# Performance work log

Measured on AMD Instinct MI355X. Metric: run time of the kernel, lower is better.

## Reference

```python
import jax, jax.numpy as jnp
import numpy as np

N_NODES = 100000
N_EDGES = 1600000
IN_F = 128
OUT_F = 32


def setup_inputs() -> dict:
    key = jax.random.key(0)
    k1, k2, k3 = jax.random.split(key, 3)
    x = jax.random.normal(k1, (N_NODES, IN_F), dtype=jnp.float32)
    edge_index = jax.random.randint(k2, (2, N_EDGES), 0, N_NODES, dtype=jnp.int64)
    W = jax.random.normal(k3, (OUT_F, IN_F), dtype=jnp.float32) * 0.1
    b = jnp.zeros((OUT_F,), dtype=jnp.float32)
    return {"x": x, "edge_index": edge_index, "W": W, "b": b}


def reference(x, edge_index, W, b):
    # PyG GCNConv: add self-loops, symmetric normalization, linear, aggregate, bias
    N = x.shape[0]
    loops = jnp.arange(N, dtype=edge_index.dtype)
    src = jnp.concatenate([edge_index[0], loops])  # message source j
    dst = jnp.concatenate([edge_index[1], loops])  # aggregation target i
    ones = jnp.ones(src.shape[0], dtype=x.dtype)
    deg = jax.ops.segment_sum(ones, dst, num_segments=N)  # deg computed at col (target)
    dis = jnp.where(deg > 0, jax.lax.rsqrt(deg), 0.0)  # deg^{-1/2}, inf -> 0
    norm = dis[src] * dis[dst]  # [E+N]
    h = x @ W.T  # [N, OUT_F] linear transform first (PyG order)
    msg = h[src] * norm[:, None]  # [E+N, OUT_F] gathered, normalized messages
    out = jax.ops.segment_sum(msg, dst, num_segments=N)  # scatter-add aggregate
    return out + b
```

## Files before the change

kernel.cpp:

```cpp
#include <hip/hip_runtime.h>

#define IN_F 128
#define OUT_F 32
#define BKT_SHIFT 9
#define BKT_NODES 512
#define NBKT 196
#define PART_CHUNK 4096
#define SORT_CAP 12288

typedef unsigned int uint32;
typedef __attribute__((ext_vector_type(8))) short bf16x8;
typedef __attribute__((ext_vector_type(4))) float f32x4;

__device__ __forceinline__ float bf2f(uint32 u) {
    union { uint32 ui; float f; } c; c.ui = u << 16; return c.f;
}
__device__ __forceinline__ uint32 f2bf(float x) {
    union { float f; uint32 ui; } c; c.f = x;
    uint32 u = c.ui;
    u += 0x7fffu + ((u >> 16) & 1u);
    return u >> 16;
}
__device__ __forceinline__ bf16x8 pack8(float4 lo, float4 hi) {
    union { bf16x8 v; uint32 u[4]; } r;
    r.u[0] = f2bf(lo.x) | (f2bf(lo.y) << 16);
    r.u[1] = f2bf(lo.z) | (f2bf(lo.w) << 16);
    r.u[2] = f2bf(hi.x) | (f2bf(hi.y) << 16);
    r.u[3] = f2bf(hi.z) | (f2bf(hi.w) << 16);
    return r.v;
}

__global__ void __launch_bounds__(256) k_phist(const int* __restrict__ dst,
        int* __restrict__ T, int E, int EB) {
    __shared__ int h[256];
    int t = threadIdx.x;
    h[t] = 0;
    __syncthreads();
    int base = blockIdx.x * PART_CHUNK;
    #pragma unroll
    for (int i = 0; i < 16; ++i) {
        int e = base + i * 256 + t;
        if (e < E) atomicAdd(&h[dst[e] >> BKT_SHIFT], 1);
    }
    __syncthreads();
    if (t < NBKT) T[t * EB + blockIdx.x] = h[t];
}

__global__ void __launch_bounds__(256) k_oscan_a(
        int* __restrict__ T, int* __restrict__ partials, int M) {
    __shared__ int sc[256];
    int t = threadIdx.x;
    int base = blockIdx.x * 512;
    int i0 = base + 2 * t, i1 = i0 + 1;
    int d0 = (i0 < M) ? T[i0] : 0;
    int d1 = (i1 < M) ? T[i1] : 0;
    sc[t] = d0 + d1;
    __syncthreads();
    #pragma unroll
    for (int ofs = 1; ofs < 256; ofs <<= 1) {
        int v = sc[t];
        int u = (t >= ofs) ? sc[t - ofs] : 0;
        __syncthreads();
        sc[t] = v + u;
        __syncthreads();
    }
    int eT = t ? sc[t - 1] : 0;
    if (i0 < M) T[i0] = eT;
    if (i1 < M) T[i1] = eT + d0;
    if (t == 0) partials[blockIdx.x] = sc[255];
}

__global__ void __launch_bounds__(256) k_oscan_b(
        const int* __restrict__ partials, int* __restrict__ bases, int nb) {
    __shared__ int sc[256];
    int t = threadIdx.x;
    sc[t] = (t < nb) ? partials[t] : 0;
    __syncthreads();
    #pragma unroll
    for (int ofs = 1; ofs < 256; ofs <<= 1) {
        int v = sc[t];
        int u = (t >= ofs) ? sc[t - ofs] : 0;
        __syncthreads();
        sc[t] = v + u;
        __syncthreads();
    }
    bases[t] = t ? sc[t - 1] : 0;
}

__global__ void k_oscan_c(int* __restrict__ T, const int* __restrict__ bases,
                          int* __restrict__ bbase, int M, int EB, int E) {
    int i = blockIdx.x * blockDim.x + threadIdx.x;
    if (i < M) {
        int v = T[i] + bases[i >> 9];
        T[i] = v;
        if (i % EB == 0) bbase[i / EB] = v;
    }
    if (i == 0) bbase[NBKT] = E;
}

__global__ void __launch_bounds__(256) k_part(
        const int* __restrict__ src, const int* __restrict__ dst,
        const int* __restrict__ T, uint32* __restrict__ pk, int E, int EB) {
    __shared__ int    hist[256];
    __shared__ int    sc[256];
    __shared__ int    cbase[256];
    __shared__ int    gbase[256];
    __shared__ uint32 stage[PART_CHUNK];
    int t = threadIdx.x;
    hist[t] = 0;
    __syncthreads();
    int base = blockIdx.x * PART_CHUNK;

    int bkt[16], rank[16];
    uint32 val[16];
    #pragma unroll
    for (int i = 0; i < 16; ++i) {
        int e = base + i * 256 + t;
        if (e < E) {
            int d = dst[e];
            int s = src[e];
            int b = d >> BKT_SHIFT;
            bkt[i] = b;
            val[i] = (uint32)s | ((uint32)(d & (BKT_NODES - 1)) << 17);
            rank[i] = atomicAdd(&hist[b], 1);
        } else {
            bkt[i] = -1;
        }
    }
    __syncthreads();
    sc[t] = hist[t];
    __syncthreads();
    #pragma unroll
    for (int ofs = 1; ofs < 256; ofs <<= 1) {
        int v = sc[t];
        int u = (t >= ofs) ? sc[t - ofs] : 0;
        __syncthreads();
        sc[t] = v + u;
        __syncthreads();
    }
    cbase[t] = t ? sc[t - 1] : 0;
    if (t < NBKT) gbase[t] = T[t * EB + blockIdx.x];
    __syncthreads();
    #pragma unroll
    for (int i = 0; i < 16; ++i)
        if (bkt[i] >= 0) stage[cbase[bkt[i]] + rank[i]] = val[i];
    __syncthreads();
    int wave = t >> 6, lane = t & 63;
    for (int b = wave; b < NBKT; b += 4) {
        int cnt_b = hist[b];
        int cb = cbase[b], gb = gbase[b];
        for (int s = lane; s < cnt_b; s += 64)
            pk[gb + s] = stage[cb + s];
    }
}

__global__ void __launch_bounds__(256) k_sort2(
        uint32* __restrict__ pk, const int* __restrict__ bbase,
        int* __restrict__ cursor, float* __restrict__ dis, int n) {
    __shared__ uint32 stg[SORT_CAP];
    __shared__ int    cnt[BKT_NODES];
    __shared__ int    sc[256];
    int b = blockIdx.x, t = threadIdx.x;
    int nodeBase = b * BKT_NODES;
    int start = bbase[b];
    int end   = bbase[b + 1];
    int len = end - start;
    for (int i = t; i < BKT_NODES; i += 256) cnt[i] = 0;
    __syncthreads();
    for (int i = t; i < len; i += 256) atomicAdd(&cnt[pk[start + i] >> 17], 1);
    __syncthreads();
    int c0 = cnt[2 * t], c1 = cnt[2 * t + 1];
    sc[t] = c0 + c1;
    __syncthreads();
    #pragma unroll
    for (int ofs = 1; ofs < 256; ofs <<= 1) {
        int v = sc[t];
        int u = (t >= ofs) ? sc[t - ofs] : 0;
        __syncthreads();
        sc[t] = v + u;
        __syncthreads();
    }
    int eT = t ? sc[t - 1] : 0;
    __syncthreads();
    cnt[2 * t]     = eT;
    cnt[2 * t + 1] = eT + c0;
    int n0 = nodeBase + 2 * t;
    if (n0 < n) {
        cursor[n0] = start + eT;
        dis[n0] = rsqrtf((float)(c0 + 1));
        int n1 = n0 + 1;
        if (n1 < n) {
            cursor[n1] = start + eT + c0;
            dis[n1] = rsqrtf((float)(c1 + 1));
        }
    }
    __syncthreads();
    for (int i = t; i < len; i += 256) {
        uint32 p = pk[start + i];
        int pos = atomicAdd(&cnt[p >> 17], 1);
        stg[pos] = p & 0x1FFFFu;
    }
    __syncthreads();
    for (int i = t; i < len; i += 256) pk[start + i] = stg[i];
}

__global__ void __launch_bounds__(256) k_gemm(
        const float* __restrict__ x, const float* __restrict__ W,
        const float* __restrict__ dis, const float* __restrict__ b,
        unsigned short* __restrict__ gbf, float* __restrict__ out, int n) {
    int lane = threadIdx.x & 63;
    int wv   = threadIdx.x >> 6;
    int nodeBase = blockIdx.x * 64 + wv * 16;
    int r16 = lane & 15;
    int kg  = lane >> 4;
    int arow = nodeBase + r16;
    if (arow >= n) arow = n - 1;
    const float4* xr = (const float4*)(x + (size_t)arow * IN_F);
    bf16x8 afr[4];
    #pragma unroll
    for (int kk = 0; kk < 4; ++kk) {
        int c4 = kk * 8 + kg * 2;
        afr[kk] = pack8(xr[c4], xr[c4 + 1]);
    }
    bf16x8 bfr[2][4];
    #pragma unroll
    for (int fb = 0; fb < 2; ++fb) {
        const float4* wr = (const float4*)(W + (size_t)(fb * 16 + r16) * IN_F);
        #pragma unroll
        for (int kk = 0; kk < 4; ++kk) {
            int c4 = kk * 8 + kg * 2;
            bfr[fb][kk] = pack8(wr[c4], wr[c4 + 1]);
        }
    }
    f32x4 acc0 = {0.f, 0.f, 0.f, 0.f};
    f32x4 acc1 = {0.f, 0.f, 0.f, 0.f};
    #pragma unroll
    for (int kk = 0; kk < 4; ++kk) {
        acc0 = __builtin_amdgcn_mfma_f32_16x16x32_bf16(afr[kk], bfr[0][kk], acc0, 0, 0, 0);
        acc1 = __builtin_amdgcn_mfma_f32_16x16x32_bf16(afr[kk], bfr[1][kk], acc1, 0, 0, 0);
    }
    float b0 = b[r16], b1 = b[16 + r16];
    #pragma unroll
    for (int j = 0; j < 4; ++j) {
        int node = nodeBase + kg * 4 + j;
        if (node < n) {
            float d = dis[node];
            float g0 = acc0[j] * d, g1 = acc1[j] * d;
            gbf[node * OUT_F + r16]      = (unsigned short)f2bf(g0);
            gbf[node * OUT_F + 16 + r16] = (unsigned short)f2bf(g1);
            out[node * OUT_F + r16]      = d * g0 + b0;
            out[node * OUT_F + 16 + r16] = d * g1 + b1;
        }
    }
}

__global__ void __launch_bounds__(256) k_aggr(
        const uint32* __restrict__ g2, const uint32* __restrict__ pk,
        const int* __restrict__ cursor, const float* __restrict__ dis,
        float* __restrict__ out, int n, int E) {
    int tid = threadIdx.x;
    int node = blockIdx.x * 16 + (tid >> 4);
    if (node >= n) return;
    int l = tid & 15;
    int start = cursor[node];
    int end   = (node + 1 < n) ? cursor[node + 1] : E;
    float ax = 0.f, ay = 0.f, bx = 0.f, by = 0.f;
    int e = start;
    for (; e + 4 <= end; e += 4) {
        int s0 = pk[e], s1 = pk[e + 1], s2 = pk[e + 2], s3 = pk[e + 3];
        uint32 v0 = g2[s0 * 16 + l];
        uint32 v1 = g2[s1 * 16 + l];
        uint32 v2 = g2[s2 * 16 + l];
        uint32 v3 = g2[s3 * 16 + l];
        ax += bf2f(v0 & 0xffffu); ay += bf2f(v0 >> 16);
        bx += bf2f(v1 & 0xffffu); by += bf2f(v1 >> 16);
        ax += bf2f(v2 & 0xffffu); ay += bf2f(v2 >> 16);
        bx += bf2f(v3 & 0xffffu); by += bf2f(v3 >> 16);
    }
    for (; e < end; ++e) {
        int s = pk[e];
        uint32 v = g2[s * 16 + l];
        ax += bf2f(v & 0xffffu); ay += bf2f(v >> 16);
    }
    float d = dis[node];
    float2* o2 = (float2*)out + (node * 16 + l);
    float2 o = *o2;
    o.x += d * (ax + bx);
    o.y += d * (ay + by);
    *o2 = o;
}

extern "C" void kernel_launch(void* const* d_in, const int* in_sizes, int n_in,
                              void* d_out, int out_size, void* d_ws, size_t ws_size,
                              hipStream_t stream) {
    const float* x  = (const float*)d_in[0];
    const int*   ei = (const int*)d_in[1];
    const float* W  = (const float*)d_in[2];
    const float* b  = (const float*)d_in[3];
    float* out = (float*)d_out;

    int N = in_sizes[0] / IN_F;
    int E = in_sizes[1] / 2;
    const int* src = ei;
    const int* dst = ei + E;

    int EB = (E + PART_CHUNK - 1) / PART_CHUNK;
    int M  = NBKT * EB;

    char* p = (char*)d_ws;
    int*            T        = (int*)p;            p += ((size_t)M * 4 + 255) & ~255ull;
    int*            partials = (int*)p;            p += 2048;
    int*            obases   = (int*)p;            p += 2048;
    int*            bbase    = (int*)p;            p += 1024;
    int*            cursor   = (int*)p;            p += ((size_t)N * 4 + 255) & ~255ull;
    float*          dis      = (float*)p;          p += ((size_t)N * 4 + 255) & ~255ull;
    uint32*         pkbuf    = (uint32*)p;         p += ((size_t)E * 4 + 255) & ~255ull;
    unsigned short* gbf      = (unsigned short*)p; p += ((size_t)N * OUT_F * 2 + 255) & ~255ull;

    int nsb = (M + 511) / 512;

    k_phist<<<EB, 256, 0, stream>>>(dst, T, E, EB);
    k_oscan_a<<<nsb, 256, 0, stream>>>(T, partials, M);
    k_oscan_b<<<1, 256, 0, stream>>>(partials, obases, nsb);
    k_oscan_c<<<(M + 255) / 256, 256, 0, stream>>>(T, obases, bbase, M, EB, E);
    k_part<<<EB, 256, 0, stream>>>(src, dst, T, pkbuf, E, EB);
    k_sort2<<<NBKT, 256, 0, stream>>>(pkbuf, bbase, cursor, dis, N);
    k_gemm<<<(N + 63) / 64, 256, 0, stream>>>(x, W, dis, b, gbf, out, N);
    k_aggr<<<(N + 15) / 16, 256, 0, stream>>>(
        (const uint32*)gbf, pkbuf, cursor, dis, out, N, E);
}
```

Measured before the change: 186.9 us.

## Merge sort and GEMM into one launch, fold scan fixup into consumers

```diff
diff --git a/kernel.cpp b/kernel.cpp
--- a/kernel.cpp
+++ b/kernel.cpp
@@ -7,6 +7,7 @@
 #define NBKT 196
 #define PART_CHUNK 4096
 #define SORT_CAP 12288
+#define GEMM_NPB 128
 
 typedef unsigned int uint32;
 typedef __attribute__((ext_vector_type(8))) short bf16x8;
@@ -30,16 +31,16 @@
     return r.v;
 }
 
-__global__ void __launch_bounds__(256) k_phist(const int* __restrict__ dst,
+__global__ void __launch_bounds__(512) k_phist(const int* __restrict__ dst,
         int* __restrict__ T, int E, int EB) {
     __shared__ int h[256];
     int t = threadIdx.x;
-    h[t] = 0;
+    if (t < 256) h[t] = 0;
     __syncthreads();
     int base = blockIdx.x * PART_CHUNK;
     #pragma unroll
-    for (int i = 0; i < 16; ++i) {
-        int e = base + i * 256 + t;
+    for (int i = 0; i < 8; ++i) {
+        int e = base + i * 512 + t;
         if (e < E) atomicAdd(&h[dst[e] >> BKT_SHIFT], 1);
     }
     __syncthreads();
@@ -87,35 +88,25 @@
     bases[t] = t ? sc[t - 1] : 0;
 }
 
-__global__ void k_oscan_c(int* __restrict__ T, const int* __restrict__ bases,
-                          int* __restrict__ bbase, int M, int EB, int E) {
-    int i = blockIdx.x * blockDim.x + threadIdx.x;
-    if (i < M) {
-        int v = T[i] + bases[i >> 9];
-        T[i] = v;
-        if (i % EB == 0) bbase[i / EB] = v;
-    }
-    if (i == 0) bbase[NBKT] = E;
-}
-
-__global__ void __launch_bounds__(256) k_part(
+__global__ void __launch_bounds__(512) k_part(
         const int* __restrict__ src, const int* __restrict__ dst,
-        const int* __restrict__ T, uint32* __restrict__ pk, int E, int EB) {
+        const int* __restrict__ T, const int* __restrict__ obases,
+        uint32* __restrict__ pk, int E, int EB) {
     __shared__ int    hist[256];
     __shared__ int    sc[256];
     __shared__ int    cbase[256];
     __shared__ int    gbase[256];
     __shared__ uint32 stage[PART_CHUNK];
     int t = threadIdx.x;
-    hist[t] = 0;
+    if (t < 256) hist[t] = 0;
     __syncthreads();
     int base = blockIdx.x * PART_CHUNK;
 
-    int bkt[16], rank[16];
-    uint32 val[16];
-    #pragma unroll
-    for (int i = 0; i < 16; ++i) {
-        int e = base + i * 256 + t;
+    int bkt[8], rank[8];
+    uint32 val[8];
+    #pragma unroll
+    for (int i = 0; i < 8; ++i) {
+        int e = base + i * 512 + t;
         if (e < E) {
             int d = dst[e];
             int s = src[e];
@@ -128,25 +119,28 @@
         }
     }
     __syncthreads();
-    sc[t] = hist[t];
+    if (t < 256) sc[t] = hist[t];
     __syncthreads();
     #pragma unroll
     for (int ofs = 1; ofs < 256; ofs <<= 1) {
-        int v = sc[t];
-        int u = (t >= ofs) ? sc[t - ofs] : 0;
-        __syncthreads();
-        sc[t] = v + u;
-        __syncthreads();
-    }
-    cbase[t] = t ? sc[t - 1] : 0;
-    if (t < NBKT) gbase[t] = T[t * EB + blockIdx.x];
-    __syncthreads();
-    #pragma unroll
-    for (int i = 0; i < 16; ++i)
+        int v = 0, u = 0;
+        if (t < 256) { v = sc[t]; u = (t >= ofs) ? sc[t - ofs] : 0; }
+        __syncthreads();
+        if (t < 256) sc[t] = v + u;
+        __syncthreads();
+    }
+    if (t < 256) cbase[t] = t ? sc[t - 1] : 0;
+    if (t < NBKT) {
+        int idx = t * EB + blockIdx.x;
+        gbase[t] = T[idx] + obases[idx >> 9];
+    }
+    __syncthreads();
+    #pragma unroll
+    for (int i = 0; i < 8; ++i)
         if (bkt[i] >= 0) stage[cbase[bkt[i]] + rank[i]] = val[i];
     __syncthreads();
     int wave = t >> 6, lane = t & 63;
-    for (int b = wave; b < NBKT; b += 4) {
+    for (int b = wave; b < NBKT; b += 8) {
         int cnt_b = hist[b];
         int cb = cbase[b], gb = gbase[b];
         for (int s = lane; s < cnt_b; s += 64)
@@ -154,102 +148,106 @@
     }
 }
 
-__global__ void __launch_bounds__(256) k_sort2(
-        uint32* __restrict__ pk, const int* __restrict__ bbase,
-        int* __restrict__ cursor, float* __restrict__ dis, int n) {
-    __shared__ uint32 stg[SORT_CAP];
-    __shared__ int    cnt[BKT_NODES];
-    __shared__ int    sc[256];
-    int b = blockIdx.x, t = threadIdx.x;
-    int nodeBase = b * BKT_NODES;
-    int start = bbase[b];
-    int end   = bbase[b + 1];
-    int len = end - start;
-    for (int i = t; i < BKT_NODES; i += 256) cnt[i] = 0;
-    __syncthreads();
-    for (int i = t; i < len; i += 256) atomicAdd(&cnt[pk[start + i] >> 17], 1);
-    __syncthreads();
-    int c0 = cnt[2 * t], c1 = cnt[2 * t + 1];
-    sc[t] = c0 + c1;
-    __syncthreads();
-    #pragma unroll
-    for (int ofs = 1; ofs < 256; ofs <<= 1) {
-        int v = sc[t];
-        int u = (t >= ofs) ? sc[t - ofs] : 0;
-        __syncthreads();
-        sc[t] = v + u;
-        __syncthreads();
-    }
-    int eT = t ? sc[t - 1] : 0;
-    __syncthreads();
-    cnt[2 * t]     = eT;
-    cnt[2 * t + 1] = eT + c0;
-    int n0 = nodeBase + 2 * t;
-    if (n0 < n) {
-        cursor[n0] = start + eT;
-        dis[n0] = rsqrtf((float)(c0 + 1));
-        int n1 = n0 + 1;
-        if (n1 < n) {
-            cursor[n1] = start + eT + c0;
-            dis[n1] = rsqrtf((float)(c1 + 1));
-        }
-    }
-    __syncthreads();
-    for (int i = t; i < len; i += 256) {
-        uint32 p = pk[start + i];
-        int pos = atomicAdd(&cnt[p >> 17], 1);
-        stg[pos] = p & 0x1FFFFu;
-    }
-    __syncthreads();
-    for (int i = t; i < len; i += 256) pk[start + i] = stg[i];
-}
-
-__global__ void __launch_bounds__(256) k_gemm(
+__global__ void __launch_bounds__(512) k_sg(
+        uint32* __restrict__ pk, const int* __restrict__ T,
+        const int* __restrict__ obases, int* __restrict__ cursor,
+        float* __restrict__ dis,
         const float* __restrict__ x, const float* __restrict__ W,
-        const float* __restrict__ dis, const float* __restrict__ b,
-        unsigned short* __restrict__ gbf, float* __restrict__ out, int n) {
-    int lane = threadIdx.x & 63;
-    int wv   = threadIdx.x >> 6;
-    int nodeBase = blockIdx.x * 64 + wv * 16;
-    int r16 = lane & 15;
-    int kg  = lane >> 4;
-    int arow = nodeBase + r16;
-    if (arow >= n) arow = n - 1;
-    const float4* xr = (const float4*)(x + (size_t)arow * IN_F);
-    bf16x8 afr[4];
-    #pragma unroll
-    for (int kk = 0; kk < 4; ++kk) {
-        int c4 = kk * 8 + kg * 2;
-        afr[kk] = pack8(xr[c4], xr[c4 + 1]);
-    }
-    bf16x8 bfr[2][4];
-    #pragma unroll
-    for (int fb = 0; fb < 2; ++fb) {
-        const float4* wr = (const float4*)(W + (size_t)(fb * 16 + r16) * IN_F);
+        unsigned short* __restrict__ gbf, int n, int E, int EB) {
+    if (blockIdx.x < NBKT) {
+        __shared__ uint32 stg[SORT_CAP];
+        __shared__ int    cnt[BKT_NODES];
+        __shared__ int    sc[256];
+        int b = blockIdx.x, t = threadIdx.x;
+        int nodeBase = b * BKT_NODES;
+        int i0 = b * EB;
+        int start = T[i0] + obases[i0 >> 9];
+        int end;
+        if (b + 1 < NBKT) {
+            int i1 = (b + 1) * EB;
+            end = T[i1] + obases[i1 >> 9];
+        } else {
+            end = E;
+        }
+        int len = end - start;
+        if (t < BKT_NODES) cnt[t] = 0;
+        __syncthreads();
+        for (int i = t; i < len; i += 512) atomicAdd(&cnt[pk[start + i] >> 17], 1);
+        __syncthreads();
+        int c0 = 0, c1 = 0;
+        if (t < 256) { c0 = cnt[2 * t]; c1 = cnt[2 * t + 1]; sc[t] = c0 + c1; }
+        __syncthreads();
+        #pragma unroll
+        for (int ofs = 1; ofs < 256; ofs <<= 1) {
+            int v = 0, u = 0;
+            if (t < 256) { v = sc[t]; u = (t >= ofs) ? sc[t - ofs] : 0; }
+            __syncthreads();
+            if (t < 256) sc[t] = v + u;
+            __syncthreads();
+        }
+        if (t < 256) {
+            int eT = t ? sc[t - 1] : 0;
+            cnt[2 * t]     = eT;
+            cnt[2 * t + 1] = eT + c0;
+            int n0 = nodeBase + 2 * t;
+            if (n0 < n) {
+                cursor[n0] = start + eT;
+                dis[n0] = rsqrtf((float)(c0 + 1));
+                int n1 = n0 + 1;
+                if (n1 < n) {
+                    cursor[n1] = start + eT + c0;
+                    dis[n1] = rsqrtf((float)(c1 + 1));
+                }
+            }
+        }
+        __syncthreads();
+        for (int i = t; i < len; i += 512) {
+            uint32 p = pk[start + i];
+            int pos = atomicAdd(&cnt[p >> 17], 1);
+            stg[pos] = p & 0x1FFFFu;
+        }
+        __syncthreads();
+        for (int i = t; i < len; i += 512) pk[start + i] = stg[i];
+    } else {
+        int gid = blockIdx.x - NBKT;
+        int lane = threadIdx.x & 63;
+        int wv   = threadIdx.x >> 6;
+        int nodeBase = gid * GEMM_NPB + wv * 16;
+        int r16 = lane & 15;
+        int kg  = lane >> 4;
+        int arow = nodeBase + r16;
+        if (arow >= n) arow = n - 1;
+        const float4* xr = (const float4*)(x + (size_t)arow * IN_F);
+        bf16x8 afr[4];
         #pragma unroll
         for (int kk = 0; kk < 4; ++kk) {
             int c4 = kk * 8 + kg * 2;
-            bfr[fb][kk] = pack8(wr[c4], wr[c4 + 1]);
-        }
-    }
-    f32x4 acc0 = {0.f, 0.f, 0.f, 0.f};
-    f32x4 acc1 = {0.f, 0.f, 0.f, 0.f};
-    #pragma unroll
-    for (int kk = 0; kk < 4; ++kk) {
-        acc0 = __builtin_amdgcn_mfma_f32_16x16x32_bf16(afr[kk], bfr[0][kk], acc0, 0, 0, 0);
-        acc1 = __builtin_amdgcn_mfma_f32_16x16x32_bf16(afr[kk], bfr[1][kk], acc1, 0, 0, 0);
-    }
-    float b0 = b[r16], b1 = b[16 + r16];
-    #pragma unroll
-    for (int j = 0; j < 4; ++j) {
-        int node = nodeBase + kg * 4 + j;
-        if (node < n) {
-            float d = dis[node];
-            float g0 = acc0[j] * d, g1 = acc1[j] * d;
-            gbf[node * OUT_F + r16]      = (unsigned short)f2bf(g0);
-            gbf[node * OUT_F + 16 + r16] = (unsigned short)f2bf(g1);
-            out[node * OUT_F + r16]      = d * g0 + b0;
-            out[node * OUT_F + 16 + r16] = d * g1 + b1;
+            afr[kk] = pack8(xr[c4], xr[c4 + 1]);
+        }
+        bf16x8 bfr[2][4];
+        #pragma unroll
+        for (int fb = 0; fb < 2; ++fb) {
+            const float4* wr = (const float4*)(W + (size_t)(fb * 16 + r16) * IN_F);
+            #pragma unroll
+            for (int kk = 0; kk < 4; ++kk) {
+                int c4 = kk * 8 + kg * 2;
+                bfr[fb][kk] = pack8(wr[c4], wr[c4 + 1]);
+            }
+        }
+        f32x4 acc0 = {0.f, 0.f, 0.f, 0.f};
+        f32x4 acc1 = {0.f, 0.f, 0.f, 0.f};
+        #pragma unroll
+        for (int kk = 0; kk < 4; ++kk) {
+            acc0 = __builtin_amdgcn_mfma_f32_16x16x32_bf16(afr[kk], bfr[0][kk], acc0, 0, 0, 0);
+            acc1 = __builtin_amdgcn_mfma_f32_16x16x32_bf16(afr[kk], bfr[1][kk], acc1, 0, 0, 0);
+        }
+        #pragma unroll
+        for (int j = 0; j < 4; ++j) {
+            int node = nodeBase + kg * 4 + j;
+            if (node < n) {
+                gbf[node * OUT_F + r16]      = (unsigned short)f2bf(acc0[j]);
+                gbf[node * OUT_F + 16 + r16] = (unsigned short)f2bf(acc1[j]);
+            }
         }
     }
 }
@@ -257,14 +255,18 @@
 __global__ void __launch_bounds__(256) k_aggr(
         const uint32* __restrict__ g2, const uint32* __restrict__ pk,
         const int* __restrict__ cursor, const float* __restrict__ dis,
-        float* __restrict__ out, int n, int E) {
+        const float* __restrict__ b, float* __restrict__ out, int n, int E) {
     int tid = threadIdx.x;
     int node = blockIdx.x * 16 + (tid >> 4);
     if (node >= n) return;
     int l = tid & 15;
     int start = cursor[node];
     int end   = (node + 1 < n) ? cursor[node + 1] : E;
-    float ax = 0.f, ay = 0.f, bx = 0.f, by = 0.f;
+    float dd = dis[node];
+    uint32 vs = g2[node * 16 + l];
+    float ax = bf2f(vs & 0xffffu) * dd;
+    float ay = bf2f(vs >> 16) * dd;
+    float bx = 0.f, by = 0.f;
     int e = start;
     for (; e + 4 <= end; e += 4) {
         int s0 = pk[e], s1 = pk[e + 1], s2 = pk[e + 2], s3 = pk[e + 3];
@@ -272,22 +274,23 @@
         uint32 v1 = g2[s1 * 16 + l];
         uint32 v2 = g2[s2 * 16 + l];
         uint32 v3 = g2[s3 * 16 + l];
-        ax += bf2f(v0 & 0xffffu); ay += bf2f(v0 >> 16);
-        bx += bf2f(v1 & 0xffffu); by += bf2f(v1 >> 16);
-        ax += bf2f(v2 & 0xffffu); ay += bf2f(v2 >> 16);
-        bx += bf2f(v3 & 0xffffu); by += bf2f(v3 >> 16);
+        float w0 = dis[s0], w1 = dis[s1], w2 = dis[s2], w3 = dis[s3];
+        ax += bf2f(v0 & 0xffffu) * w0; ay += bf2f(v0 >> 16) * w0;
+        bx += bf2f(v1 & 0xffffu) * w1; by += bf2f(v1 >> 16) * w1;
+        ax += bf2f(v2 & 0xffffu) * w2; ay += bf2f(v2 >> 16) * w2;
+        bx += bf2f(v3 & 0xffffu) * w3; by += bf2f(v3 >> 16) * w3;
     }
     for (; e < end; ++e) {
         int s = pk[e];
         uint32 v = g2[s * 16 + l];
-        ax += bf2f(v & 0xffffu); ay += bf2f(v >> 16);
-    }
-    float d = dis[node];
-    float2* o2 = (float2*)out + (node * 16 + l);
-    float2 o = *o2;
-    o.x += d * (ax + bx);
-    o.y += d * (ay + by);
-    *o2 = o;
+        float w = dis[s];
+        ax += bf2f(v & 0xffffu) * w; ay += bf2f(v >> 16) * w;
+    }
+    float2 bb = ((const float2*)b)[l];
+    float2 o;
+    o.x = dd * (ax + bx) + bb.x;
+    o.y = dd * (ay + by) + bb.y;
+    ((float2*)out)[node * 16 + l] = o;
 }
 
 extern "C" void kernel_launch(void* const* d_in, const int* in_sizes, int n_in,
@@ -311,21 +314,20 @@
     int*            T        = (int*)p;            p += ((size_t)M * 4 + 255) & ~255ull;
     int*            partials = (int*)p;            p += 2048;
     int*            obases   = (int*)p;            p += 2048;
-    int*            bbase    = (int*)p;            p += 1024;
     int*            cursor   = (int*)p;            p += ((size_t)N * 4 + 255) & ~255ull;
     float*          dis      = (float*)p;          p += ((size_t)N * 4 + 255) & ~255ull;
     uint32*         pkbuf    = (uint32*)p;         p += ((size_t)E * 4 + 255) & ~255ull;
     unsigned short* gbf      = (unsigned short*)p; p += ((size_t)N * OUT_F * 2 + 255) & ~255ull;
 
     int nsb = (M + 511) / 512;
-
-    k_phist<<<EB, 256, 0, stream>>>(dst, T, E, EB);
+    int gemmBlocks = (N + GEMM_NPB - 1) / GEMM_NPB;
+
+    k_phist<<<EB, 512, 0, stream>>>(dst, T, E, EB);
     k_oscan_a<<<nsb, 256, 0, stream>>>(T, partials, M);
     k_oscan_b<<<1, 256, 0, stream>>>(partials, obases, nsb);
-    k_oscan_c<<<(M + 255) / 256, 256, 0, stream>>>(T, obases, bbase, M, EB, E);
-    k_part<<<EB, 256, 0, stream>>>(src, dst, T, pkbuf, E, EB);
-    k_sort2<<<NBKT, 256, 0, stream>>>(pkbuf, bbase, cursor, dis, N);
-    k_gemm<<<(N + 63) / 64, 256, 0, stream>>>(x, W, dis, b, gbf, out, N);
+    k_part<<<EB, 512, 0, stream>>>(src, dst, T, obases, pkbuf, E, EB);
+    k_sg<<<NBKT + gemmBlocks, 512, 0, stream>>>(
+        pkbuf, T, obases, cursor, dis, x, W, gbf, N, E, EB);
     k_aggr<<<(N + 15) / 16, 256, 0, stream>>>(
-        (const uint32*)gbf, pkbuf, cursor, dis, out, N, E);
-}
+        (const uint32*)gbf, pkbuf, cursor, dis, b, out, N, E);
+}
```

Measured after the change: 162.2 us. 13.2% less time.
